# Kernel optimization log

Measured on AMD Instinct MI355X. Metric: run time of the kernel, lower is better.

Reference implementation:

```python
import jax, jax.numpy as jnp
import numpy as np

SQ, B, H = 2048, 1, 4096
NP, HN, MQG = 32, 128, 2          # query heads, head_dim, kv groups
ROT = HN // 2                      # rotary dim = 64 (partial rotary)
NORM = float(np.sqrt(HN))


def apply_rope(x, rope):
    # x: [sq, b, nh, hn]; rope: [sq, 1, ROT//2, 2] (cos, sin)
    sq, b, nh, hn = x.shape
    rot = rope.shape[-2] * 2
    xr, xp = x[..., :rot], x[..., rot:]
    xs = xr.reshape(sq, b, nh, rot // 2, 2)
    rc = rope[:sq].reshape(sq, -1, 1, rot // 2, 2)
    o0 = xs[..., 0] * rc[..., 0] - xs[..., 1] * rc[..., 1]
    o1 = xs[..., 1] * rc[..., 0] + xs[..., 0] * rc[..., 1]
    out = jnp.stack([o0, o1], -1).reshape(sq, b, nh, rot)
    return jnp.concatenate([out, xp], axis=-1)


def setup_inputs() -> dict:
    key = jax.random.key(0)
    k0, k1, k2, k3 = jax.random.split(key, 4)
    qkv_dim = NP * HN + 2 * MQG * HN  # 4608
    hidden_states = jax.random.normal(k0, (SQ, B, H), jnp.float32) * 0.02
    Wqkv = jax.random.normal(k1, (qkv_dim, H), jnp.float32) * 0.02
    bqkv = jax.random.normal(k2, (qkv_dim,), jnp.float32) * 0.02
    Wdense = jax.random.normal(k3, (H, NP * HN), jnp.float32) * 0.02
    # rope cache [sq, 1, ROT//2, 2]
    pos = jnp.arange(SQ, dtype=jnp.float32)
    inv = 1.0 / (10000.0 ** (jnp.arange(0, ROT, 2, dtype=jnp.float32) / ROT))
    ang = pos[:, None] * inv[None, :]
    rotary_pos_emb = jnp.stack([jnp.cos(ang), jnp.sin(ang)], -1)[:, None, :, :]
    # additive causal mask [b, 1, sq, sq]
    causal = jnp.tril(jnp.ones((SQ, SQ), bool))
    attention_mask = jnp.broadcast_to(
        jnp.where(causal, 0.0, -1e9).astype(jnp.float32), (B, 1, SQ, SQ))
    return dict(hidden_states=hidden_states, Wqkv=Wqkv, bqkv=bqkv,
                Wdense=Wdense, rotary_pos_emb=rotary_pos_emb,
                attention_mask=attention_mask)


def reference(hidden_states, Wqkv, bqkv, Wdense, rotary_pos_emb, attention_mask):
    sq, b, _ = hidden_states.shape
    mixed = hidden_states @ Wqkv.T + bqkv            # [sq, b, 4608]
    qd, kvd = NP * HN, MQG * HN
    q = mixed[..., :qd].reshape(sq, b, NP, HN)
    k = mixed[..., qd:qd + kvd].reshape(sq, b, MQG, HN)
    v = mixed[..., qd + kvd:].reshape(sq, b, MQG, HN)
    q = apply_rope(q, rotary_pos_emb)
    k = apply_rope(k, rotary_pos_emb)
    # -> [b, heads, sq, hn]
    q = q.transpose(1, 2, 0, 3)
    k = k.transpose(1, 2, 0, 3)
    v = v.transpose(1, 2, 0, 3)
    # MQA grouping: q [b, g, n_rep, sq, hn]; kv kept at [b, g, sq, hn]
    n_rep = NP // MQG
    qg = q.reshape(b, MQG, n_rep, sq, HN)
    scores = jnp.einsum('bgrqd,bgkd->bgrqk', qg, k) / NORM
    scores = scores + attention_mask[:, None]        # [b,1,1,sq,sq] broadcast
    probs = jax.nn.softmax(scores.astype(jnp.float32), axis=-1).astype(q.dtype)
    ctx = jnp.einsum('bgrqk,bgkd->bgrqd', probs, v)  # [b, g, n_rep, sq, hn]
    ctx = ctx.reshape(b, NP, sq, HN).transpose(0, 2, 1, 3).reshape(b, sq, NP * HN)
    out = ctx @ Wdense.T                             # [b, sq, H]
    return out
```

## Files before the change

kernel.cpp:

```cpp
#include <hip/hip_runtime.h>
#include <stdint.h>

#define SQL 2048
#define HID 4096
#define NHEADS 32
#define HDSZ 128
#define QKVD 4608
#define QDIM 4096

typedef unsigned short u16;
typedef __attribute__((ext_vector_type(8))) short short8;
typedef __attribute__((ext_vector_type(4))) float f32x4;

#define AS1(p) ((__attribute__((address_space(1))) void*)(p))
#define AS3(p) ((__attribute__((address_space(3))) void*)(p))

__device__ __forceinline__ float bf2f(u16 u) {
  return __uint_as_float(((uint32_t)u) << 16);
}
__device__ __forceinline__ u16 f2bf(float f) {
  uint32_t x = __float_as_uint(f);
  x += 0x7fffu + ((x >> 16) & 1u);
  return (u16)(x >> 16);
}

__global__ void k_cvt(const float* __restrict__ in, u16* __restrict__ out, int n8) {
  int i = blockIdx.x * blockDim.x + threadIdx.x;
  int stride = gridDim.x * blockDim.x;
  for (; i < n8; i += stride) {
    const float4* p = reinterpret_cast<const float4*>(in) + (size_t)i * 2;
    float4 a = p[0], b = p[1];
    short8 o;
    o[0] = (short)f2bf(a.x); o[1] = (short)f2bf(a.y);
    o[2] = (short)f2bf(a.z); o[3] = (short)f2bf(a.w);
    o[4] = (short)f2bf(b.x); o[5] = (short)f2bf(b.y);
    o[6] = (short)f2bf(b.z); o[7] = (short)f2bf(b.w);
    reinterpret_cast<short8*>(out)[i] = o;
  }
}

template<int MODE>
__global__ __launch_bounds__(256, 2)
void k_gemm(const u16* __restrict__ A, const u16* __restrict__ B,
            const float* __restrict__ bias,
            u16* __restrict__ qbuf, u16* __restrict__ kbuf, u16* __restrict__ vtbuf,
            float* __restrict__ outf)
{
  __shared__ __align__(16) u16 ldsA[128 * 64];
  __shared__ __align__(16) u16 ldsB[128 * 64];
  const int tid = threadIdx.x;
  const int wid = tid >> 6, lane = tid & 63;
  const int l15 = lane & 15, lg = lane >> 4;
  const int m0 = blockIdx.y * 128, n0 = blockIdx.x * 128;
  const int wr = wid >> 1, wc = wid & 1;

  f32x4 acc[4][4] = {};

  const int srow = lane >> 3;
  const int skb  = (((lane & 7) ^ srow) << 4);
  const size_t rowbytes = (size_t)HID * 2;

  for (int t = 0; t < HID / 64; ++t) {
    __syncthreads();
    const char* Ab = (const char*)A + (size_t)m0 * rowbytes + (size_t)t * 128;
    const char* Bb = (const char*)B + (size_t)n0 * rowbytes + (size_t)t * 128;
#pragma unroll
    for (int i = 0; i < 4; ++i) {
      int seg = i * 4 + wid;
      int row = seg * 8 + srow;
      __builtin_amdgcn_global_load_lds(AS1(Ab + (size_t)row * rowbytes + skb),
                                       AS3(ldsA + seg * 512), 16, 0, 0);
      __builtin_amdgcn_global_load_lds(AS1(Bb + (size_t)row * rowbytes + skb),
                                       AS3(ldsB + seg * 512), 16, 0, 0);
    }
    __syncthreads();
#pragma unroll
    for (int kc = 0; kc < 2; ++kc) {
      short8 af[4], bfr[4];
#pragma unroll
      for (int mi = 0; mi < 4; ++mi) {
        int row = wr * 64 + mi * 16 + l15;
        int kb = (kc * 64 + lg * 16) ^ ((row & 7) << 4);
        af[mi] = *reinterpret_cast<const short8*>((const char*)ldsA + row * 128 + kb);
      }
#pragma unroll
      for (int ni = 0; ni < 4; ++ni) {
        int row = wc * 64 + ni * 16 + l15;
        int kb = (kc * 64 + lg * 16) ^ ((row & 7) << 4);
        bfr[ni] = *reinterpret_cast<const short8*>((const char*)ldsB + row * 128 + kb);
      }
#pragma unroll
      for (int mi = 0; mi < 4; ++mi)
#pragma unroll
        for (int ni = 0; ni < 4; ++ni)
          acc[mi][ni] = __builtin_amdgcn_mfma_f32_16x16x32_bf16(af[mi], bfr[ni], acc[mi][ni], 0, 0, 0);
    }
  }

#pragma unroll
  for (int mi = 0; mi < 4; ++mi) {
#pragma unroll
    for (int ni = 0; ni < 4; ++ni) {
      int row0 = m0 + wr * 64 + mi * 16 + lg * 4;
      int col  = n0 + wc * 64 + ni * 16 + l15;
      if (MODE == 0) {
        float bv = bias[col];
#pragma unroll
        for (int j = 0; j < 4; ++j) {
          float v = acc[mi][ni][j] + bv;
          int r = row0 + j;
          if (col < QDIM) {
            v *= 0.08838834764831845f;
            int hh = col >> 7, d = col & 127;
            qbuf[((size_t)hh * SQL + r) * HDSZ + d] = f2bf(v);
          } else if (col < QDIM + 256) {
            int c2 = col - QDIM; int g = c2 >> 7, d = c2 & 127;
            kbuf[((size_t)g * SQL + r) * HDSZ + d] = f2bf(v);
          } else {
            int c2 = col - QDIM - 256; int g = c2 >> 7, d = c2 & 127;
            vtbuf[((size_t)g * HDSZ + d) * SQL + r] = f2bf(v);
          }
        }
      } else {
#pragma unroll
        for (int j = 0; j < 4; ++j)
          outf[(size_t)(row0 + j) * QDIM + col] = acc[mi][ni][j];
      }
    }
  }
}

__global__ void k_rope(u16* __restrict__ qbuf, u16* __restrict__ kbuf,
                       const float* __restrict__ rope) {
  int idx = blockIdx.x * blockDim.x + threadIdx.x;
  if (idx >= SQL * 34 * 32) return;
  int p = idx & 31;
  int hh = (idx >> 5) % 34;
  int s = idx / (34 * 32);
  float c  = rope[s * 64 + p * 2 + 0];
  float sn = rope[s * 64 + p * 2 + 1];
  u16* base = (hh < 32) ? (qbuf + ((size_t)hh * SQL + s) * HDSZ)
                        : (kbuf + ((size_t)(hh - 32) * SQL + s) * HDSZ);
  u16* pp = base + 2 * p;
  uint32_t packed = *reinterpret_cast<uint32_t*>(pp);
  float x0 = bf2f((u16)(packed & 0xffff));
  float x1 = bf2f((u16)(packed >> 16));
  float o0 = x0 * c - x1 * sn;
  float o1 = x1 * c + x0 * sn;
  *reinterpret_cast<uint32_t*>(pp) = (uint32_t)f2bf(o0) | ((uint32_t)f2bf(o1) << 16);
}

__global__ __launch_bounds__(64)
void k_attn(const u16* __restrict__ qbuf, const u16* __restrict__ kbuf,
            const u16* __restrict__ vtbuf, u16* __restrict__ ctx)
{
  __shared__ uint32_t plw[32][36];
  const int lane = threadIdx.x;
  const int l15 = lane & 15, lg = lane >> 4;
  const int h = blockIdx.x;
  const int g = h >> 4;
  const int qi = (int)gridDim.y - 1 - (int)blockIdx.y;
  const int q0 = qi * 32;

  short8 aq[2][4];
#pragma unroll
  for (int rt = 0; rt < 2; ++rt) {
    const u16* qp = qbuf + ((size_t)h * SQL + q0 + rt * 16 + l15) * HDSZ + lg * 8;
#pragma unroll
    for (int kc = 0; kc < 4; ++kc)
      aq[rt][kc] = *reinterpret_cast<const short8*>(qp + kc * 32);
  }
  f32x4 o[2][8] = {};
  float mrow[2], lrow[2];
#pragma unroll
  for (int rt = 0; rt < 2; ++rt) { mrow[rt] = -__builtin_inff(); lrow[rt] = 0.f; }

  const int jend = q0 + 31;
  for (int j0 = 0; j0 <= jend; j0 += 64) {
    short8 bk[4][4];
    const u16* kp = kbuf + ((size_t)g * SQL + j0 + l15) * HDSZ + lg * 8;
#pragma unroll
    for (int kt = 0; kt < 4; ++kt)
#pragma unroll
      for (int kc = 0; kc < 4; ++kc)
        bk[kt][kc] = *reinterpret_cast<const short8*>(kp + (size_t)kt * 16 * HDSZ + kc * 32);

    f32x4 st[2][4] = {};
    __builtin_amdgcn_s_setprio(1);
#pragma unroll
    for (int kc = 0; kc < 4; ++kc)
#pragma unroll
      for (int rt = 0; rt < 2; ++rt)
#pragma unroll
        for (int kt = 0; kt < 4; ++kt)
          st[rt][kt] = __builtin_amdgcn_mfma_f32_16x16x32_bf16(bk[kt][kc], aq[rt][kc], st[rt][kt], 0, 0, 0);
    __builtin_amdgcn_s_setprio(0);

    short8 bv[8][2];
    const u16* vp = vtbuf + ((size_t)g * HDSZ + l15) * SQL + j0 + lg * 8;
#pragma unroll
    for (int df = 0; df < 8; ++df)
#pragma unroll
      for (int kc2 = 0; kc2 < 2; ++kc2)
        bv[df][kc2] = *reinterpret_cast<const short8*>(vp + (size_t)df * 16 * SQL + kc2 * 32);

    const bool domask = (j0 + 63 > q0);
#pragma unroll
    for (int rt = 0; rt < 2; ++rt) {
      const int q = q0 + rt * 16 + l15;
      float p[4][4];
#pragma unroll
      for (int kt = 0; kt < 4; ++kt)
#pragma unroll
        for (int j = 0; j < 4; ++j) {
          float v = st[rt][kt][j];
          if (domask) {
            int kvi = j0 + kt * 16 + lg * 4 + j;
            v = (kvi > q) ? -1e30f : v;
          }
          p[kt][j] = v;
        }
      float rm = fmaxf(fmaxf(fmaxf(p[0][0], p[0][1]), fmaxf(p[0][2], p[0][3])),
                       fmaxf(fmaxf(p[1][0], p[1][1]), fmaxf(p[1][2], p[1][3])));
      rm = fmaxf(rm, fmaxf(fmaxf(fmaxf(p[2][0], p[2][1]), fmaxf(p[2][2], p[2][3])),
                           fmaxf(fmaxf(p[3][0], p[3][1]), fmaxf(p[3][2], p[3][3]))));
      rm = fmaxf(rm, __shfl_xor(rm, 16));
      rm = fmaxf(rm, __shfl_xor(rm, 32));
      if (!__all(rm <= mrow[rt] + 8.0f)) {
        float mn = fmaxf(mrow[rt], rm);
        float a = __expf(mrow[rt] - mn);
        mrow[rt] = mn;
        lrow[rt] *= a;
        float ar[4];
#pragma unroll
        for (int j = 0; j < 4; ++j) ar[j] = __shfl(a, lg * 4 + j);
#pragma unroll
        for (int df = 0; df < 8; ++df) {
          o[rt][df][0] *= ar[0]; o[rt][df][1] *= ar[1];
          o[rt][df][2] *= ar[2]; o[rt][df][3] *= ar[3];
        }
      }
      float ps = 0.f;
#pragma unroll
      for (int kt = 0; kt < 4; ++kt)
#pragma unroll
        for (int j = 0; j < 4; ++j) {
          p[kt][j] = __expf(p[kt][j] - mrow[rt]);
          ps += p[kt][j];
        }
      ps += __shfl_xor(ps, 16);
      ps += __shfl_xor(ps, 32);
      lrow[rt] += ps;
#pragma unroll
      for (int kt = 0; kt < 4; ++kt)
#pragma unroll
        for (int u = 0; u < 2; ++u) {
          uint32_t W;
          asm("v_cvt_pk_bf16_f32 %0, %1, %2"
              : "=v"(W) : "v"(p[kt][2 * u]), "v"(p[kt][2 * u + 1]));
          plw[rt * 16 + l15][8 * kt + 2 * lg + u] = W;
        }
    }
    asm volatile("s_waitcnt lgkmcnt(0)" ::: "memory");

    short8 ap[2][2];
#pragma unroll
    for (int rt = 0; rt < 2; ++rt)
#pragma unroll
      for (int kc2 = 0; kc2 < 2; ++kc2)
        ap[rt][kc2] = *reinterpret_cast<const short8*>(&plw[rt * 16 + l15][16 * kc2 + 4 * lg]);

    __builtin_amdgcn_s_setprio(1);
#pragma unroll
    for (int rt = 0; rt < 2; ++rt) {
#pragma unroll
      for (int df = 0; df < 8; ++df) {
        f32x4 t = o[rt][df];
        t = __builtin_amdgcn_mfma_f32_16x16x32_bf16(ap[rt][0], bv[df][0], t, 0, 0, 0);
        t = __builtin_amdgcn_mfma_f32_16x16x32_bf16(ap[rt][1], bv[df][1], t, 0, 0, 0);
        o[rt][df] = t;
      }
    }
    __builtin_amdgcn_s_setprio(0);
  }

#pragma unroll
  for (int rt = 0; rt < 2; ++rt) {
    float linv[4];
#pragma unroll
    for (int j = 0; j < 4; ++j) linv[j] = 1.0f / __shfl(lrow[rt], lg * 4 + j);
#pragma unroll
    for (int j = 0; j < 4; ++j) {
      int row = q0 + rt * 16 + lg * 4 + j;
      u16* cp = ctx + (size_t)row * QDIM + h * HDSZ;
#pragma unroll
      for (int df = 0; df < 8; ++df)
        cp[df * 16 + l15] = f2bf(o[rt][df][j] * linv[j]);
    }
  }
}


extern "C" void kernel_launch(void* const* d_in, const int* in_sizes, int n_in,
                              void* d_out, int out_size, void* d_ws, size_t ws_size,
                              hipStream_t stream) {
  const float* hs     = (const float*)d_in[0];
  const float* wqkv   = (const float*)d_in[1];
  const float* bqkv   = (const float*)d_in[2];
  const float* wdense = (const float*)d_in[3];
  const float* rope   = (const float*)d_in[4];
  char* ws = (char*)d_ws;
  u16* hid_b = (u16*)(ws + 0);
  u16* w_b   = (u16*)(ws + 16777216);
  u16* qb    = (u16*)(ws + 54525952);
  u16* kb    = (u16*)(ws + 71303168);
  u16* vtb   = (u16*)(ws + 72351744);
  u16* ctx   = hid_b;
  float* outf = (float*)d_out;

  k_cvt<<<2048, 256, 0, stream>>>(hs,   hid_b, SQL * HID / 8);
  k_cvt<<<2048, 256, 0, stream>>>(wqkv, w_b,   QKVD * HID / 8);
  k_gemm<0><<<dim3(QKVD / 128, SQL / 128), 256, 0, stream>>>(
      hid_b, w_b, bqkv, qb, kb, vtb, nullptr);
  k_rope<<<(SQL * 34 * 32) / 256, 256, 0, stream>>>(qb, kb, rope);
  k_cvt<<<2048, 256, 0, stream>>>(wdense, w_b, QDIM * HID / 8);
  k_attn<<<dim3(NHEADS, SQL / 32), 64, 0, stream>>>(qb, kb, vtb, ctx);
  k_gemm<1><<<dim3(QDIM / 128, SQL / 128), 256, 0, stream>>>(
      ctx, w_b, nullptr, nullptr, nullptr, nullptr, outf);
}
```

Measured before the change: 335.0 us.

## Share K/V tiles across 8 waves via double-buffered LDS in attention

Restructures the attention kernel from one 64-thread wave per 32-query block to 512-thread blocks where 8 waves (query blocks spaced 256 apart) share K and V tiles staged into swizzled, double-buffered LDS with global_load_lds. This cuts redundant global/L2 reads of K and V, which each wave previously fetched independently, and balances causal work by interleaving query blocks. In exchange, all waves iterate to the longest wave's range with __syncthreads each tile, so short-range waves idle. It also raises LDS use and drops the grid to 256 blocks.

```diff
diff --git a/kernel.cpp b/kernel.cpp
--- a/kernel.cpp
+++ b/kernel.cpp
@@ -150,17 +150,43 @@
   *reinterpret_cast<uint32_t*>(pp) = (uint32_t)f2bf(o0) | ((uint32_t)f2bf(o1) << 16);
 }
 
-__global__ __launch_bounds__(64)
+__global__ __launch_bounds__(512, 2)
 void k_attn(const u16* __restrict__ qbuf, const u16* __restrict__ kbuf,
             const u16* __restrict__ vtbuf, u16* __restrict__ ctx)
 {
-  __shared__ uint32_t plw[32][36];
-  const int lane = threadIdx.x;
+  __shared__ __align__(16) u16 KL[2][64 * 128];
+  __shared__ __align__(16) u16 VL[2][128 * 64];
+  __shared__ uint32_t plw[8][32][36];
+  const int tid = threadIdx.x;
+  const int wid = tid >> 6, lane = tid & 63;
   const int l15 = lane & 15, lg = lane >> 4;
   const int h = blockIdx.x;
   const int g = h >> 4;
-  const int qi = (int)gridDim.y - 1 - (int)blockIdx.y;
-  const int q0 = qi * 32;
+  const int bq = blockIdx.y;
+  const int q0 = wid * 256 + bq * 32;
+  const int ext = q0 + 32;
+  const int NT = (1824 + 32 * bq + 63) >> 6;
+
+  const int cA = tid, cB = tid + 512;
+  const int krA = cA >> 4, kiA = (cA & 15) ^ (krA & 7);
+  const int krB = cB >> 4, kiB = (cB & 15) ^ (krB & 7);
+  const int vrA = cA >> 3, viA = (cA & 7) ^ (vrA & 7);
+  const int vrB = cB >> 3, viB = (cB & 7) ^ (vrB & 7);
+  const char* kg = (const char*)(kbuf + (size_t)g * SQL * HDSZ);
+  const char* vg = (const char*)(vtbuf + (size_t)g * HDSZ * SQL);
+
+#define STAGE(t, b)                                                             \
+  do {                                                                          \
+    int j0s = (t) * 64;                                                         \
+    __builtin_amdgcn_global_load_lds(AS1(kg + (size_t)(j0s + krA) * 256 + (kiA << 4)), \
+                                     AS3((char*)KL[b] + cA * 16), 16, 0, 0);    \
+    __builtin_amdgcn_global_load_lds(AS1(kg + (size_t)(j0s + krB) * 256 + (kiB << 4)), \
+                                     AS3((char*)KL[b] + cB * 16), 16, 0, 0);    \
+    __builtin_amdgcn_global_load_lds(AS1(vg + (size_t)vrA * (SQL * 2) + j0s * 2 + (viA << 4)), \
+                                     AS3((char*)VL[b] + cA * 16), 16, 0, 0);    \
+    __builtin_amdgcn_global_load_lds(AS1(vg + (size_t)vrB * (SQL * 2) + j0s * 2 + (viB << 4)), \
+                                     AS3((char*)VL[b] + cB * 16), 16, 0, 0);    \
+  } while (0)
 
   short8 aq[2][4];
 #pragma unroll
@@ -175,113 +201,126 @@
 #pragma unroll
   for (int rt = 0; rt < 2; ++rt) { mrow[rt] = -__builtin_inff(); lrow[rt] = 0.f; }
 
-  const int jend = q0 + 31;
-  for (int j0 = 0; j0 <= jend; j0 += 64) {
-    short8 bk[4][4];
-    const u16* kp = kbuf + ((size_t)g * SQL + j0 + l15) * HDSZ + lg * 8;
-#pragma unroll
-    for (int kt = 0; kt < 4; ++kt)
-#pragma unroll
-      for (int kc = 0; kc < 4; ++kc)
-        bk[kt][kc] = *reinterpret_cast<const short8*>(kp + (size_t)kt * 16 * HDSZ + kc * 32);
-
-    f32x4 st[2][4] = {};
-    __builtin_amdgcn_s_setprio(1);
-#pragma unroll
-    for (int kc = 0; kc < 4; ++kc)
+  STAGE(0, 0);
+  __syncthreads();
+
+  for (int i = 0; i < NT; ++i) {
+    const int cur = i & 1;
+    if (i + 1 < NT) STAGE(i + 1, cur ^ 1);
+
+    const int j0 = i * 64;
+    if (j0 < ext) {
+      const char* kb0 = (const char*)KL[cur];
+      const char* vb0 = (const char*)VL[cur];
+      const int swz = (l15 & 7) << 4;
+
+      f32x4 st[2][4] = {};
+#pragma unroll
+      for (int kc = 0; kc < 4; ++kc) {
+        short8 bk4[4];
+#pragma unroll
+        for (int kt = 0; kt < 4; ++kt) {
+          int r = 16 * kt + l15;
+          bk4[kt] = *reinterpret_cast<const short8*>(
+              kb0 + r * 256 + ((kc * 64 + lg * 16) ^ swz));
+        }
+        __builtin_amdgcn_s_setprio(1);
+#pragma unroll
+        for (int rt = 0; rt < 2; ++rt)
+#pragma unroll
+          for (int kt = 0; kt < 4; ++kt)
+            st[rt][kt] = __builtin_amdgcn_mfma_f32_16x16x32_bf16(bk4[kt], aq[rt][kc], st[rt][kt], 0, 0, 0);
+        __builtin_amdgcn_s_setprio(0);
+      }
+
+      const bool domask = (j0 + 63 > q0);
+#pragma unroll
+      for (int rt = 0; rt < 2; ++rt) {
+        const int q = q0 + rt * 16 + l15;
+        float p[4][4];
+#pragma unroll
+        for (int kt = 0; kt < 4; ++kt)
+#pragma unroll
+          for (int j = 0; j < 4; ++j) {
+            float v = st[rt][kt][j];
+            if (domask) {
+              int kvi = j0 + kt * 16 + lg * 4 + j;
+              v = (kvi > q) ? -1e30f : v;
+            }
+            p[kt][j] = v;
+          }
+        float rm = fmaxf(fmaxf(fmaxf(p[0][0], p[0][1]), fmaxf(p[0][2], p[0][3])),
+                         fmaxf(fmaxf(p[1][0], p[1][1]), fmaxf(p[1][2], p[1][3])));
+        rm = fmaxf(rm, fmaxf(fmaxf(fmaxf(p[2][0], p[2][1]), fmaxf(p[2][2], p[2][3])),
+                             fmaxf(fmaxf(p[3][0], p[3][1]), fmaxf(p[3][2], p[3][3]))));
+        rm = fmaxf(rm, __shfl_xor(rm, 16));
+        rm = fmaxf(rm, __shfl_xor(rm, 32));
+        if (!__all(rm <= mrow[rt] + 8.0f)) {
+          float mn = fmaxf(mrow[rt], rm);
+          float a = __expf(mrow[rt] - mn);
+          mrow[rt] = mn;
+          lrow[rt] *= a;
+          float ar[4];
+#pragma unroll
+          for (int j = 0; j < 4; ++j) ar[j] = __shfl(a, lg * 4 + j);
+#pragma unroll
+          for (int df = 0; df < 8; ++df) {
+            o[rt][df][0] *= ar[0]; o[rt][df][1] *= ar[1];
+            o[rt][df][2] *= ar[2]; o[rt][df][3] *= ar[3];
+          }
+        }
+        float ps = 0.f;
+#pragma unroll
+        for (int kt = 0; kt < 4; ++kt)
+#pragma unroll
+          for (int j = 0; j < 4; ++j) {
+            p[kt][j] = __expf(p[kt][j] - mrow[rt]);
+            ps += p[kt][j];
+          }
+        ps += __shfl_xor(ps, 16);
+        ps += __shfl_xor(ps, 32);
+        lrow[rt] += ps;
+#pragma unroll
+        for (int kt = 0; kt < 4; ++kt)
+#pragma unroll
+          for (int u = 0; u < 2; ++u) {
+            uint32_t W;
+            asm("v_cvt_pk_bf16_f32 %0, %1, %2"
+                : "=v"(W) : "v"(p[kt][2 * u]), "v"(p[kt][2 * u + 1]));
+            plw[wid][rt * 16 + l15][8 * kt + 2 * lg + u] = W;
+          }
+      }
+      asm volatile("s_waitcnt lgkmcnt(0)" ::: "memory");
+
+      short8 ap[2][2];
 #pragma unroll
       for (int rt = 0; rt < 2; ++rt)
 #pragma unroll
-        for (int kt = 0; kt < 4; ++kt)
-          st[rt][kt] = __builtin_amdgcn_mfma_f32_16x16x32_bf16(bk[kt][kc], aq[rt][kc], st[rt][kt], 0, 0, 0);
-    __builtin_amdgcn_s_setprio(0);
-
-    short8 bv[8][2];
-    const u16* vp = vtbuf + ((size_t)g * HDSZ + l15) * SQL + j0 + lg * 8;
-#pragma unroll
-    for (int df = 0; df < 8; ++df)
-#pragma unroll
-      for (int kc2 = 0; kc2 < 2; ++kc2)
-        bv[df][kc2] = *reinterpret_cast<const short8*>(vp + (size_t)df * 16 * SQL + kc2 * 32);
-
-    const bool domask = (j0 + 63 > q0);
-#pragma unroll
-    for (int rt = 0; rt < 2; ++rt) {
-      const int q = q0 + rt * 16 + l15;
-      float p[4][4];
-#pragma unroll
-      for (int kt = 0; kt < 4; ++kt)
-#pragma unroll
-        for (int j = 0; j < 4; ++j) {
-          float v = st[rt][kt][j];
-          if (domask) {
-            int kvi = j0 + kt * 16 + lg * 4 + j;
-            v = (kvi > q) ? -1e30f : v;
-          }
-          p[kt][j] = v;
-        }
-      float rm = fmaxf(fmaxf(fmaxf(p[0][0], p[0][1]), fmaxf(p[0][2], p[0][3])),
-                       fmaxf(fmaxf(p[1][0], p[1][1]), fmaxf(p[1][2], p[1][3])));
-      rm = fmaxf(rm, fmaxf(fmaxf(fmaxf(p[2][0], p[2][1]), fmaxf(p[2][2], p[2][3])),
-                           fmaxf(fmaxf(p[3][0], p[3][1]), fmaxf(p[3][2], p[3][3]))));
-      rm = fmaxf(rm, __shfl_xor(rm, 16));
-      rm = fmaxf(rm, __shfl_xor(rm, 32));
-      if (!__all(rm <= mrow[rt] + 8.0f)) {
-        float mn = fmaxf(mrow[rt], rm);
-        float a = __expf(mrow[rt] - mn);
-        mrow[rt] = mn;
-        lrow[rt] *= a;
-        float ar[4];
-#pragma unroll
-        for (int j = 0; j < 4; ++j) ar[j] = __shfl(a, lg * 4 + j);
-#pragma unroll
-        for (int df = 0; df < 8; ++df) {
-          o[rt][df][0] *= ar[0]; o[rt][df][1] *= ar[1];
-          o[rt][df][2] *= ar[2]; o[rt][df][3] *= ar[3];
-        }
-      }
-      float ps = 0.f;
-#pragma unroll
-      for (int kt = 0; kt < 4; ++kt)
-#pragma unroll
-        for (int j = 0; j < 4; ++j) {
-          p[kt][j] = __expf(p[kt][j] - mrow[rt]);
-          ps += p[kt][j];
-        }
-      ps += __shfl_xor(ps, 16);
-      ps += __shfl_xor(ps, 32);
-      lrow[rt] += ps;
-#pragma unroll
-      for (int kt = 0; kt < 4; ++kt)
-#pragma unroll
-        for (int u = 0; u < 2; ++u) {
-          uint32_t W;
-          asm("v_cvt_pk_bf16_f32 %0, %1, %2"
-              : "=v"(W) : "v"(p[kt][2 * u]), "v"(p[kt][2 * u + 1]));
-          plw[rt * 16 + l15][8 * kt + 2 * lg + u] = W;
-        }
-    }
-    asm volatile("s_waitcnt lgkmcnt(0)" ::: "memory");
-
-    short8 ap[2][2];
-#pragma unroll
-    for (int rt = 0; rt < 2; ++rt)
-#pragma unroll
-      for (int kc2 = 0; kc2 < 2; ++kc2)
-        ap[rt][kc2] = *reinterpret_cast<const short8*>(&plw[rt * 16 + l15][16 * kc2 + 4 * lg]);
-
-    __builtin_amdgcn_s_setprio(1);
-#pragma unroll
-    for (int rt = 0; rt < 2; ++rt) {
+        for (int kc2 = 0; kc2 < 2; ++kc2)
+          ap[rt][kc2] = *reinterpret_cast<const short8*>(&plw[wid][rt * 16 + l15][16 * kc2 + 4 * lg]);
+
+      __builtin_amdgcn_s_setprio(1);
 #pragma unroll
       for (int df = 0; df < 8; ++df) {
-        f32x4 t = o[rt][df];
-        t = __builtin_amdgcn_mfma_f32_16x16x32_bf16(ap[rt][0], bv[df][0], t, 0, 0, 0);
-        t = __builtin_amdgcn_mfma_f32_16x16x32_bf16(ap[rt][1], bv[df][1], t, 0, 0, 0);
-        o[rt][df] = t;
-      }
-    }
-    __builtin_amdgcn_s_setprio(0);
+        short8 bv0, bv1;
+        int rv = l15 + 16 * df;
+#pragma unroll
+        for (int kc2 = 0; kc2 < 2; ++kc2) {
+          short8 bvv = *reinterpret_cast<const short8*>(
+              vb0 + rv * 128 + ((kc2 * 64 + lg * 16) ^ swz));
+          if (kc2 == 0) bv0 = bvv; else bv1 = bvv;
+        }
+#pragma unroll
+        for (int rt = 0; rt < 2; ++rt) {
+          f32x4 t = o[rt][df];
+          t = __builtin_amdgcn_mfma_f32_16x16x32_bf16(ap[rt][0], bv0, t, 0, 0, 0);
+          t = __builtin_amdgcn_mfma_f32_16x16x32_bf16(ap[rt][1], bv1, t, 0, 0, 0);
+          o[rt][df] = t;
+        }
+      }
+      __builtin_amdgcn_s_setprio(0);
+    }
+    __syncthreads();
   }
 
 #pragma unroll
@@ -298,6 +337,7 @@
         cp[df * 16 + l15] = f2bf(o[rt][df][j] * linv[j]);
     }
   }
+#undef STAGE
 }
 
 
@@ -324,7 +364,7 @@
       hid_b, w_b, bqkv, qb, kb, vtb, nullptr);
   k_rope<<<(SQL * 34 * 32) / 256, 256, 0, stream>>>(qb, kb, rope);
   k_cvt<<<2048, 256, 0, stream>>>(wdense, w_b, QDIM * HID / 8);
-  k_attn<<<dim3(NHEADS, SQL / 32), 64, 0, stream>>>(qb, kb, vtb, ctx);
+  k_attn<<<dim3(NHEADS, 8), 512, 0, stream>>>(qb, kb, vtb, ctx);
   k_gemm<1><<<dim3(QDIM / 128, SQL / 128), 256, 0, stream>>>(
       ctx, w_b, nullptr, nullptr, nullptr, nullptr, outf);
 }
```

Result: faster. 302.3 us (median of 2 runs) (-9.8%).
